# Performance work log

Hardware: AMD Instinct MI355X
Metric: run time of the kernel (lower is better)

Reference implementation:

```python
import jax, jax.numpy as jnp
import numpy as np

N_NODES = 50000
N_EDGES = 800000
D_IN = 96
D_EDGE = 32
D_OUT = 96
N_TYPES = 4


def setup_inputs() -> dict:
    key = jax.random.key(0)
    k = jax.random.split(key, 6)
    x = jax.random.normal(k[0], (N_NODES, D_IN), dtype=jnp.float32)
    edge_features = jax.random.normal(k[1], (N_NODES, D_EDGE), dtype=jnp.float32)
    edge_index = jax.random.randint(k[2], (2, N_EDGES), 0, N_NODES, dtype=jnp.int32)
    edge_type = jax.random.randint(k[3], (N_EDGES,), 0, N_TYPES, dtype=jnp.int32)
    # One RelEdgeConv per relation type: Linear(D_IN + D_EDGE -> D_OUT) message fn
    scale = 1.0 / np.sqrt(D_IN + D_EDGE)
    W_msg = jax.random.uniform(k[4], (N_TYPES, D_IN + D_EDGE, D_OUT), jnp.float32, -scale, scale)
    b_msg = jax.random.uniform(k[5], (N_TYPES, D_OUT), jnp.float32, -scale, scale)
    return {"x": x, "edge_features": edge_features, "edge_index": edge_index,
            "edge_type": edge_type, "W_msg": W_msg, "b_msg": b_msg}


def reference(x, edge_features, edge_index, edge_type, W_msg, b_msg):
    # Node-level edge_features (shape[0] == N) -> per-edge relative features
    src, dst = edge_index[0], edge_index[1]
    e = jnp.abs(edge_features[src] - edge_features[dst])          # [E, De]
    feat = jnp.concatenate([x[src], e], axis=-1)                  # [E, Din+De]
    n_nodes = x.shape[0]
    n_types = W_msg.shape[0]

    def per_type(t):
        # relation mask: zero out messages for edges of other types
        mask = (edge_type == t).astype(x.dtype)[:, None]          # [E, 1]
        m = (feat @ W_msg[t] + b_msg[t]) * mask                   # [E, Dout]
        # scatter-add messages to destination nodes
        return jax.ops.segment_sum(m, dst, num_segments=n_nodes)  # [N, Dout]

    out = jnp.stack([per_type(t) for t in range(n_types)])        # [T, N, Dout]
    return out.mean(axis=0)
```

## Files before the change

kernel.cpp:

```cpp
#include <hip/hip_runtime.h>

#define E_EDGES 800000
#define NN 50000
#define D_IN 96
#define D_EDGE 32
#define D_OUT 96
#define KSUM 512
#define SSTRIDE 520
#define NB2 782
#define BCAP2 1216
#define NCHUNK 256
#define CHE 3125
#define CHIT 13
#define BUILD_BLOCKS 512

typedef __attribute__((ext_vector_type(8))) __bf16 bf16x8;
typedef __attribute__((ext_vector_type(4))) float floatx4;

__device__ __forceinline__ float lo16(unsigned int u) {
    return __builtin_bit_cast(float, u << 16);
}
__device__ __forceinline__ float hi16(unsigned int u) {
    return __builtin_bit_cast(float, u & 0xFFFF0000u);
}
__device__ __forceinline__ unsigned int pk2(float a, float b) {
    unsigned short ua = __builtin_bit_cast(unsigned short, (__bf16)a);
    unsigned short ub = __builtin_bit_cast(unsigned short, (__bf16)b);
    return (unsigned int)ua | ((unsigned int)ub << 16);
}

__global__ __launch_bounds__(256) void k_prep(const int* __restrict__ ei,
                                              const int* __restrict__ et,
                                              const float* __restrict__ x,
                                              const float* __restrict__ ef,
                                              const float* __restrict__ Wm,
                                              int* __restrict__ cursor,
                                              int* __restrict__ eb,
                                              __bf16* __restrict__ WT,
                                              unsigned int* __restrict__ xeb) {
    __shared__ int lcnt[NB2];
    __shared__ int gb[NB2];
    int tid = threadIdx.x, bid = blockIdx.x;

    if (bid < NCHUNK) {
        int e0 = bid * CHE;
        for (int i = tid; i < NB2; i += 256) lcnt[i] = 0;
        __syncthreads();

        int pv[CHIT], br[CHIT];
#pragma unroll
        for (int it = 0; it < CHIT; it++) {
            int i = it * 256 + tid;
            br[it] = -1;
            if (i < CHE) {
                int e = e0 + i;
                int dst = ei[E_EDGES + e];
                int b = dst >> 6;
                int rank = atomicAdd(&lcnt[b], 1);
                pv[it] = (ei[e] << 6) | (et[e] << 22) | ((dst & 63) << 24);
                br[it] = rank | (b << 16);
            }
        }
        __syncthreads();
        for (int b = tid; b < NB2; b += 256)
            gb[b] = lcnt[b] ? atomicAdd(&cursor[b], lcnt[b]) : 0;
        __syncthreads();
#pragma unroll
        for (int it = 0; it < CHIT; it++) {
            if (br[it] >= 0) {
                int b = br[it] >> 16, rank = br[it] & 0xFFFF;
                int pos = gb[b] + rank;
                if (pos < BCAP2) eb[b * BCAP2 + pos] = pv[it];
            }
        }
    } else {
        int b2 = bid - NCHUNK;
        int gtid = b2 * 256 + tid;
        int lane = tid & 63, w = tid >> 6;
        for (int n = b2 * 4 + w; n < NN; n += BUILD_BLOCKS * 4) {
            float2 v;
            if (lane < 48) v = *(const float2*)(x  + (size_t)n * D_IN   + 2 * lane);
            else           v = *(const float2*)(ef + (size_t)n * D_EDGE + 2 * (lane - 48));
            xeb[(size_t)n * 64 + lane] = pk2(v.x, v.y);
        }
        for (int i = gtid; i < 96 * KSUM; i += BUILD_BLOCKS * 256) {
            int n = i >> 9, k = i & 511;
            WT[n * KSUM + k] = (__bf16)Wm[(size_t)k * 96 + n];
        }
    }
}

__global__ __launch_bounds__(256) void k_fused(const int* __restrict__ cursor,
                                               const int* __restrict__ eb,
                                               const unsigned int* __restrict__ xeb,
                                               const __bf16* __restrict__ WT,
                                               const float* __restrict__ bm,
                                               float* __restrict__ out) {
    __shared__ int ecopy[BCAP2];
    __shared__ int elist[BCAP2];
    __shared__ int h[256], hbase[256], c2[256];
    __shared__ __align__(16) __bf16 Sl[16][SSTRIDE];

    int tid = threadIdx.x, lane = tid & 63, w = tid >> 6;
    int B = blockIdx.x;
    int seg = B * BCAP2;
    int m = min(cursor[B], BCAP2);

    h[tid] = 0;
    __syncthreads();

    for (int i = tid; i < m; i += 256) {
        int p = eb[seg + i];
        ecopy[i] = p;
        atomicAdd(&h[(p >> 22) & 255], 1);
    }
    __syncthreads();

    int v = h[tid];
    c2[tid] = v; __syncthreads();
    for (int d = 1; d < 256; d <<= 1) {
        int t = (tid >= d) ? c2[tid - d] : 0;
        __syncthreads();
        c2[tid] += t; __syncthreads();
    }
    hbase[tid] = c2[tid] - v;
    c2[tid] = c2[tid] - v;
    __syncthreads();

    for (int i = tid; i < m; i += 256) {
        int p = ecopy[i];
        int pos = atomicAdd(&c2[(p >> 22) & 255], 1);
        elist[pos] = p;
    }
    __syncthreads();

    unsigned int Mmask = (lane >= 48) ? 0x7FFFFFFFu : 0xFFFFFFFFu;

#define ACCS(u, v) do {                                                        \
        float f0 = lo16(u), f1 = hi16(u);                                      \
        f0 = __builtin_bit_cast(float,                                         \
                 __builtin_bit_cast(unsigned int, f0 - e0) & Mmask);           \
        f1 = __builtin_bit_cast(float,                                         \
                 __builtin_bit_cast(unsigned int, f1 - e1) & Mmask);           \
        int sty = (__builtin_amdgcn_readfirstlane(v) >> 22) & 3;               \
        if      (sty == 0) { s0a += f0; s0b += f1; }                           \
        else if (sty == 1) { s1a += f0; s1b += f1; }                           \
        else if (sty == 2) { s2a += f0; s2b += f1; }                           \
        else               { s3a += f0; s3b += f1; }                           \
    } while (0)

    int quad = lane >> 4, low = lane & 15;

    for (int c4 = 0; c4 < 4; c4++) {
        for (int j = 0; j < 4; j++) {
            int lr = w * 4 + j;
            int nl = c4 * 16 + lr;
            int n = B * 64 + nl;
            int bs = hbase[nl * 4];
            int num = h[nl * 4] + h[nl * 4 + 1] + h[nl * 4 + 2] + h[nl * 4 + 3];
            float s0a = 0, s0b = 0, s1a = 0, s1b = 0,
                  s2a = 0, s2b = 0, s3a = 0, s3b = 0;
            float e0 = 0.f, e1 = 0.f;
            if (lane >= 48 && num > 0) {
                unsigned int u = xeb[(size_t)n * 64 + lane];
                e0 = lo16(u); e1 = hi16(u);
            }

            int i = 0;
            for (; i + 7 < num; i += 8) {
                int v0 = elist[bs + i],     v1 = elist[bs + i + 1];
                int v2 = elist[bs + i + 2], v3 = elist[bs + i + 3];
                int v4 = elist[bs + i + 4], v5 = elist[bs + i + 5];
                int v6 = elist[bs + i + 6], v7 = elist[bs + i + 7];
                unsigned int u0 = xeb[(v0 & 0x3FFFFF) + lane];
                unsigned int u1 = xeb[(v1 & 0x3FFFFF) + lane];
                unsigned int u2 = xeb[(v2 & 0x3FFFFF) + lane];
                unsigned int u3 = xeb[(v3 & 0x3FFFFF) + lane];
                unsigned int u4 = xeb[(v4 & 0x3FFFFF) + lane];
                unsigned int u5 = xeb[(v5 & 0x3FFFFF) + lane];
                unsigned int u6 = xeb[(v6 & 0x3FFFFF) + lane];
                unsigned int u7 = xeb[(v7 & 0x3FFFFF) + lane];
                ACCS(u0, v0); ACCS(u1, v1); ACCS(u2, v2); ACCS(u3, v3);
                ACCS(u4, v4); ACCS(u5, v5); ACCS(u6, v6); ACCS(u7, v7);
            }
            for (; i < num; i++) {
                int vv = elist[bs + i];
                unsigned int u = xeb[(vv & 0x3FFFFF) + lane];
                ACCS(u, vv);
            }

            unsigned int* sp = (unsigned int*)&Sl[lr][0];
            sp[  0 + lane] = pk2(s0a, s0b);
            sp[ 64 + lane] = pk2(s1a, s1b);
            sp[128 + lane] = pk2(s2a, s2b);
            sp[192 + lane] = pk2(s3a, s3b);
        }
        __syncthreads();

        bf16x8 a[16];
        const __bf16* ap = &Sl[low][0] + quad * 8;
#pragma unroll
        for (int ks = 0; ks < 16; ks++) a[ks] = *(const bf16x8*)(ap + ks * 32);

        for (int ct = w; ct < 6; ct += 4) {
            floatx4 acc = {0.f, 0.f, 0.f, 0.f};
            const __bf16* bp = WT + (size_t)(ct * 16 + low) * KSUM + quad * 8;
#pragma unroll
            for (int ks = 0; ks < 16; ks++)
                acc = __builtin_amdgcn_mfma_f32_16x16x32_bf16(
                    a[ks], *(const bf16x8*)(bp + ks * 32), acc, 0, 0, 0);
            int col = ct * 16 + low;
#pragma unroll
            for (int rg = 0; rg < 4; rg++) {
                int r = quad * 4 + rg;
                int nl = c4 * 16 + r;
                int g = B * 64 + nl;
                if (g < NN) {
                    float bias = (float)h[nl * 4 + 0] * bm[col]
                               + (float)h[nl * 4 + 1] * bm[96 + col]
                               + (float)h[nl * 4 + 2] * bm[192 + col]
                               + (float)h[nl * 4 + 3] * bm[288 + col];
                    out[(size_t)g * D_OUT + col] = 0.25f * (acc[rg] + bias);
                }
            }
        }
        __syncthreads();
    }
#undef ACCS
}

extern "C" void kernel_launch(void* const* d_in, const int* in_sizes, int n_in,
                              void* d_out, int out_size, void* d_ws, size_t ws_size,
                              hipStream_t stream) {
    const float* x  = (const float*)d_in[0];
    const float* ef = (const float*)d_in[1];
    const int*   ei = (const int*)d_in[2];
    const int*   et = (const int*)d_in[3];
    const float* Wm = (const float*)d_in[4];
    const float* bm = (const float*)d_in[5];
    float* out = (float*)d_out;

    int* cursor = (int*)d_ws;
    int* eb     = cursor + 1024;
    __bf16* WT  = (__bf16*)(eb + NB2 * BCAP2);
    unsigned int* xeb = (unsigned int*)(WT + 96 * KSUM);

    hipMemsetAsync(cursor, 0, NB2 * sizeof(int), stream);
    k_prep <<<NCHUNK + BUILD_BLOCKS, 256, 0, stream>>>(ei, et, x, ef, Wm,
                                                       cursor, eb, WT, xeb);
    k_fused<<<NB2, 256, 0, stream>>>(cursor, eb, xeb, WT, bm, out);
}
```

Baseline: 208.4 us.

## Halve destination bucket size and stage scattered edge writes through shared memory

Destination buckets shrink from 64 to 32 nodes, so the fused kernel launches twice as many blocks, each with a smaller edge list and two 16-row MFMA chunks instead of four. This raises parallelism and occupancy for the gather/aggregate phase. The prep kernel now does a block-local prefix scan over bucket counts and stages edges in shared memory so the global writes to the bucket array are grouped. A 4-wide unrolled tail loop is added to the gather. The extra shared memory in prep (two arrays of CHE ints) may lower occupancy for the prep and build blocks, and the per-bucket capacity of 704 could drop edges if a 32-node bucket overflows.

```diff
diff --git a/kernel.cpp b/kernel.cpp
--- a/kernel.cpp
+++ b/kernel.cpp
@@ -7,12 +7,13 @@
 #define D_OUT 96
 #define KSUM 512
 #define SSTRIDE 520
-#define NB2 782
-#define BCAP2 1216
+#define NB3 1564
+#define BCAP3 704
 #define NCHUNK 256
 #define CHE 3125
 #define CHIT 13
 #define BUILD_BLOCKS 512
+#define SPT 7
 
 typedef __attribute__((ext_vector_type(8))) __bf16 bf16x8;
 typedef __attribute__((ext_vector_type(4))) float floatx4;
@@ -38,13 +39,17 @@
                                               int* __restrict__ eb,
                                               __bf16* __restrict__ WT,
                                               unsigned int* __restrict__ xeb) {
-    __shared__ int lcnt[NB2];
-    __shared__ int gb[NB2];
+    __shared__ int lcnt[NB3];
+    __shared__ int lexcl[NB3];
+    __shared__ int gb[NB3];
+    __shared__ int tmp[256];
+    __shared__ int stage[CHE];
+    __shared__ int spos[CHE];
     int tid = threadIdx.x, bid = blockIdx.x;
 
     if (bid < NCHUNK) {
         int e0 = bid * CHE;
-        for (int i = tid; i < NB2; i += 256) lcnt[i] = 0;
+        for (int i = tid; i < NB3; i += 256) lcnt[i] = 0;
         __syncthreads();
 
         int pv[CHIT], br[CHIT];
@@ -55,23 +60,50 @@
             if (i < CHE) {
                 int e = e0 + i;
                 int dst = ei[E_EDGES + e];
-                int b = dst >> 6;
+                int b = dst >> 5;
                 int rank = atomicAdd(&lcnt[b], 1);
-                pv[it] = (ei[e] << 6) | (et[e] << 22) | ((dst & 63) << 24);
+                pv[it] = (ei[e] << 6) | (et[e] << 22) | ((dst & 31) << 24);
                 br[it] = rank | (b << 16);
             }
         }
         __syncthreads();
-        for (int b = tid; b < NB2; b += 256)
+        {
+            int s = 0;
+#pragma unroll
+            for (int k = 0; k < SPT; k++) {
+                int idx = tid * SPT + k;
+                if (idx < NB3) { lexcl[idx] = s; s += lcnt[idx]; }
+            }
+            tmp[tid] = s; __syncthreads();
+            for (int d = 1; d < 256; d <<= 1) {
+                int t = (tid >= d) ? tmp[tid - d] : 0;
+                __syncthreads();
+                tmp[tid] += t; __syncthreads();
+            }
+            int base = tmp[tid] - s;
+#pragma unroll
+            for (int k = 0; k < SPT; k++) {
+                int idx = tid * SPT + k;
+                if (idx < NB3) lexcl[idx] += base;
+            }
+        }
+        for (int b = tid; b < NB3; b += 256)
             gb[b] = lcnt[b] ? atomicAdd(&cursor[b], lcnt[b]) : 0;
         __syncthreads();
 #pragma unroll
         for (int it = 0; it < CHIT; it++) {
             if (br[it] >= 0) {
                 int b = br[it] >> 16, rank = br[it] & 0xFFFF;
-                int pos = gb[b] + rank;
-                if (pos < BCAP2) eb[b * BCAP2 + pos] = pv[it];
-            }
+                int lidx = lexcl[b] + rank;
+                stage[lidx] = pv[it];
+                int gp = gb[b] + rank;
+                spos[lidx] = (gp < BCAP3) ? (b * BCAP3 + gp) : -1;
+            }
+        }
+        __syncthreads();
+        for (int i = tid; i < CHE; i += 256) {
+            int p = spos[i];
+            if (p >= 0) eb[p] = stage[i];
         }
     } else {
         int b2 = bid - NCHUNK;
@@ -96,40 +128,40 @@
                                                const __bf16* __restrict__ WT,
                                                const float* __restrict__ bm,
                                                float* __restrict__ out) {
-    __shared__ int ecopy[BCAP2];
-    __shared__ int elist[BCAP2];
-    __shared__ int h[256], hbase[256], c2[256];
+    __shared__ int ecopy[BCAP3];
+    __shared__ int elist[BCAP3];
+    __shared__ int h[128], hbase[128], c2[256];
     __shared__ __align__(16) __bf16 Sl[16][SSTRIDE];
 
     int tid = threadIdx.x, lane = tid & 63, w = tid >> 6;
     int B = blockIdx.x;
-    int seg = B * BCAP2;
-    int m = min(cursor[B], BCAP2);
-
-    h[tid] = 0;
+    int seg = B * BCAP3;
+    int m = min(cursor[B], BCAP3);
+
+    if (tid < 128) h[tid] = 0;
     __syncthreads();
 
     for (int i = tid; i < m; i += 256) {
         int p = eb[seg + i];
         ecopy[i] = p;
-        atomicAdd(&h[(p >> 22) & 255], 1);
-    }
-    __syncthreads();
-
-    int v = h[tid];
+        atomicAdd(&h[(p >> 22) & 127], 1);
+    }
+    __syncthreads();
+
+    int v = (tid < 128) ? h[tid] : 0;
     c2[tid] = v; __syncthreads();
     for (int d = 1; d < 256; d <<= 1) {
         int t = (tid >= d) ? c2[tid - d] : 0;
         __syncthreads();
         c2[tid] += t; __syncthreads();
     }
-    hbase[tid] = c2[tid] - v;
+    if (tid < 128) { hbase[tid] = c2[tid] - v; }
     c2[tid] = c2[tid] - v;
     __syncthreads();
 
     for (int i = tid; i < m; i += 256) {
         int p = ecopy[i];
-        int pos = atomicAdd(&c2[(p >> 22) & 255], 1);
+        int pos = atomicAdd(&c2[(p >> 22) & 127], 1);
         elist[pos] = p;
     }
     __syncthreads();
@@ -151,11 +183,11 @@
 
     int quad = lane >> 4, low = lane & 15;
 
-    for (int c4 = 0; c4 < 4; c4++) {
+    for (int ch = 0; ch < 2; ch++) {
         for (int j = 0; j < 4; j++) {
             int lr = w * 4 + j;
-            int nl = c4 * 16 + lr;
-            int n = B * 64 + nl;
+            int nl = ch * 16 + lr;
+            int n = B * 32 + nl;
             int bs = hbase[nl * 4];
             int num = h[nl * 4] + h[nl * 4 + 1] + h[nl * 4 + 2] + h[nl * 4 + 3];
             float s0a = 0, s0b = 0, s1a = 0, s1b = 0,
@@ -183,6 +215,15 @@
                 ACCS(u0, v0); ACCS(u1, v1); ACCS(u2, v2); ACCS(u3, v3);
                 ACCS(u4, v4); ACCS(u5, v5); ACCS(u6, v6); ACCS(u7, v7);
             }
+            for (; i + 3 < num; i += 4) {
+                int v0 = elist[bs + i],     v1 = elist[bs + i + 1];
+                int v2 = elist[bs + i + 2], v3 = elist[bs + i + 3];
+                unsigned int u0 = xeb[(v0 & 0x3FFFFF) + lane];
+                unsigned int u1 = xeb[(v1 & 0x3FFFFF) + lane];
+                unsigned int u2 = xeb[(v2 & 0x3FFFFF) + lane];
+                unsigned int u3 = xeb[(v3 & 0x3FFFFF) + lane];
+                ACCS(u0, v0); ACCS(u1, v1); ACCS(u2, v2); ACCS(u3, v3);
+            }
             for (; i < num; i++) {
                 int vv = elist[bs + i];
                 unsigned int u = xeb[(vv & 0x3FFFFF) + lane];
@@ -213,8 +254,8 @@
 #pragma unroll
             for (int rg = 0; rg < 4; rg++) {
                 int r = quad * 4 + rg;
-                int nl = c4 * 16 + r;
-                int g = B * 64 + nl;
+                int nl = ch * 16 + r;
+                int g = B * 32 + nl;
                 if (g < NN) {
                     float bias = (float)h[nl * 4 + 0] * bm[col]
                                + (float)h[nl * 4 + 1] * bm[96 + col]
@@ -241,12 +282,12 @@
     float* out = (float*)d_out;
 
     int* cursor = (int*)d_ws;
-    int* eb     = cursor + 1024;
-    __bf16* WT  = (__bf16*)(eb + NB2 * BCAP2);
+    int* eb     = cursor + 2048;
+    __bf16* WT  = (__bf16*)(eb + NB3 * BCAP3);
     unsigned int* xeb = (unsigned int*)(WT + 96 * KSUM);
 
-    hipMemsetAsync(cursor, 0, NB2 * sizeof(int), stream);
+    hipMemsetAsync(cursor, 0, NB3 * sizeof(int), stream);
     k_prep <<<NCHUNK + BUILD_BLOCKS, 256, 0, stream>>>(ei, et, x, ef, Wm,
                                                        cursor, eb, WT, xeb);
-    k_fused<<<NB2, 256, 0, stream>>>(cursor, eb, xeb, WT, bm, out);
-}
+    k_fused<<<NB3, 256, 0, stream>>>(cursor, eb, xeb, WT, bm, out);
+}
```

Result: faster. 202.4 us (-2.9%).

## Shrink destination buckets to 16 nodes and gather per-type edge runs

Applied to the files above, without the earlier changes.

Destination buckets shrink from 64 to 16 nodes, so the fused kernel launches 3125 blocks instead of 782. Each block runs a single MFMA tile pass instead of four. The 256-entry block scan becomes a 64-lane wavefront shuffle scan. The gather loop walks each (node, type) run on its own, dropping the readfirstlane type branch, and uses a 4-wide masked unroll that clamps out-of-range elist reads. This aims at more parallelism and less divergent per-edge branching, at the cost of more blocks, more bucket atomics and per-block WT reloads, and a lower bucket capacity (384) that could overflow on skewed degree distributions.

```diff
diff --git a/kernel.cpp b/kernel.cpp
--- a/kernel.cpp
+++ b/kernel.cpp
@@ -7,8 +7,8 @@
 #define D_OUT 96
 #define KSUM 512
 #define SSTRIDE 520
-#define NB2 782
-#define BCAP2 1216
+#define NB4 3125
+#define BCAP4 384
 #define NCHUNK 256
 #define CHE 3125
 #define CHIT 13
@@ -38,13 +38,13 @@
                                               int* __restrict__ eb,
                                               __bf16* __restrict__ WT,
                                               unsigned int* __restrict__ xeb) {
-    __shared__ int lcnt[NB2];
-    __shared__ int gb[NB2];
+    __shared__ int lcnt[NB4];
+    __shared__ int gb[NB4];
     int tid = threadIdx.x, bid = blockIdx.x;
 
     if (bid < NCHUNK) {
         int e0 = bid * CHE;
-        for (int i = tid; i < NB2; i += 256) lcnt[i] = 0;
+        for (int i = tid; i < NB4; i += 256) lcnt[i] = 0;
         __syncthreads();
 
         int pv[CHIT], br[CHIT];
@@ -55,14 +55,14 @@
             if (i < CHE) {
                 int e = e0 + i;
                 int dst = ei[E_EDGES + e];
-                int b = dst >> 6;
+                int b = dst >> 4;
                 int rank = atomicAdd(&lcnt[b], 1);
-                pv[it] = (ei[e] << 6) | (et[e] << 22) | ((dst & 63) << 24);
+                pv[it] = (ei[e] << 6) | (et[e] << 22) | ((dst & 15) << 24);
                 br[it] = rank | (b << 16);
             }
         }
         __syncthreads();
-        for (int b = tid; b < NB2; b += 256)
+        for (int b = tid; b < NB4; b += 256)
             gb[b] = lcnt[b] ? atomicAdd(&cursor[b], lcnt[b]) : 0;
         __syncthreads();
 #pragma unroll
@@ -70,7 +70,7 @@
             if (br[it] >= 0) {
                 int b = br[it] >> 16, rank = br[it] & 0xFFFF;
                 int pos = gb[b] + rank;
-                if (pos < BCAP2) eb[b * BCAP2 + pos] = pv[it];
+                if (pos < BCAP4) eb[b * BCAP4 + pos] = pv[it];
             }
         }
     } else {
@@ -96,137 +96,117 @@
                                                const __bf16* __restrict__ WT,
                                                const float* __restrict__ bm,
                                                float* __restrict__ out) {
-    __shared__ int ecopy[BCAP2];
-    __shared__ int elist[BCAP2];
-    __shared__ int h[256], hbase[256], c2[256];
+    __shared__ int ecopy[BCAP4];
+    __shared__ int elist[BCAP4];
+    __shared__ int h[64], hbase[64];
+    __shared__ int c2[64];
     __shared__ __align__(16) __bf16 Sl[16][SSTRIDE];
 
     int tid = threadIdx.x, lane = tid & 63, w = tid >> 6;
     int B = blockIdx.x;
-    int seg = B * BCAP2;
-    int m = min(cursor[B], BCAP2);
-
-    h[tid] = 0;
+    int seg = B * BCAP4;
+    int m = min(cursor[B], BCAP4);
+
+    if (tid < 64) h[tid] = 0;
     __syncthreads();
 
     for (int i = tid; i < m; i += 256) {
         int p = eb[seg + i];
         ecopy[i] = p;
-        atomicAdd(&h[(p >> 22) & 255], 1);
-    }
-    __syncthreads();
-
-    int v = h[tid];
-    c2[tid] = v; __syncthreads();
-    for (int d = 1; d < 256; d <<= 1) {
-        int t = (tid >= d) ? c2[tid - d] : 0;
-        __syncthreads();
-        c2[tid] += t; __syncthreads();
-    }
-    hbase[tid] = c2[tid] - v;
-    c2[tid] = c2[tid] - v;
+        atomicAdd(&h[(p >> 22) & 63], 1);
+    }
+    __syncthreads();
+
+    if (w == 0) {
+        int v = h[lane];
+        int s = v;
+        for (int d = 1; d < 64; d <<= 1) {
+            int t = __shfl_up(s, d, 64);
+            if (lane >= d) s += t;
+        }
+        hbase[lane] = s - v;
+        c2[lane] = s - v;
+    }
     __syncthreads();
 
     for (int i = tid; i < m; i += 256) {
         int p = ecopy[i];
-        int pos = atomicAdd(&c2[(p >> 22) & 255], 1);
+        int pos = atomicAdd(&c2[(p >> 22) & 63], 1);
         elist[pos] = p;
     }
     __syncthreads();
 
     unsigned int Mmask = (lane >= 48) ? 0x7FFFFFFFu : 0xFFFFFFFFu;
-
-#define ACCS(u, v) do {                                                        \
-        float f0 = lo16(u), f1 = hi16(u);                                      \
+    int quad = lane >> 4, low = lane & 15;
+
+#define EDGE(k) do {                                                           \
+        float f0 = lo16(u##k), f1 = hi16(u##k);                                \
         f0 = __builtin_bit_cast(float,                                         \
                  __builtin_bit_cast(unsigned int, f0 - e0) & Mmask);           \
         f1 = __builtin_bit_cast(float,                                         \
                  __builtin_bit_cast(unsigned int, f1 - e1) & Mmask);           \
-        int sty = (__builtin_amdgcn_readfirstlane(v) >> 22) & 3;               \
-        if      (sty == 0) { s0a += f0; s0b += f1; }                           \
-        else if (sty == 1) { s1a += f0; s1b += f1; }                           \
-        else if (sty == 2) { s2a += f0; s2b += f1; }                           \
-        else               { s3a += f0; s3b += f1; }                           \
+        sa += (i + k < num) ? f0 : 0.f;                                        \
+        sb += (i + k < num) ? f1 : 0.f;                                        \
     } while (0)
 
-    int quad = lane >> 4, low = lane & 15;
-
-    for (int c4 = 0; c4 < 4; c4++) {
-        for (int j = 0; j < 4; j++) {
-            int lr = w * 4 + j;
-            int nl = c4 * 16 + lr;
-            int n = B * 64 + nl;
-            int bs = hbase[nl * 4];
-            int num = h[nl * 4] + h[nl * 4 + 1] + h[nl * 4 + 2] + h[nl * 4 + 3];
-            float s0a = 0, s0b = 0, s1a = 0, s1b = 0,
-                  s2a = 0, s2b = 0, s3a = 0, s3b = 0;
-            float e0 = 0.f, e1 = 0.f;
-            if (lane >= 48 && num > 0) {
-                unsigned int u = xeb[(size_t)n * 64 + lane];
-                e0 = lo16(u); e1 = hi16(u);
-            }
-
-            int i = 0;
-            for (; i + 7 < num; i += 8) {
-                int v0 = elist[bs + i],     v1 = elist[bs + i + 1];
-                int v2 = elist[bs + i + 2], v3 = elist[bs + i + 3];
-                int v4 = elist[bs + i + 4], v5 = elist[bs + i + 5];
-                int v6 = elist[bs + i + 6], v7 = elist[bs + i + 7];
+    for (int j = 0; j < 4; j++) {
+        int nl = w * 4 + j;
+        int n = B * 16 + nl;
+        float e0 = 0.f, e1 = 0.f;
+        if (lane >= 48) {
+            unsigned int u = xeb[(size_t)n * 64 + lane];
+            e0 = lo16(u); e1 = hi16(u);
+        }
+        unsigned int* sp = (unsigned int*)&Sl[nl][0];
+
+#pragma unroll
+        for (int t = 0; t < 4; t++) {
+            int bs = hbase[nl * 4 + t];
+            int num = h[nl * 4 + t];
+            float sa = 0.f, sb = 0.f;
+            for (int i = 0; i < num; i += 4) {
+                int i1 = bs + i + 1, i2 = bs + i + 2, i3 = bs + i + 3;
+                int lim = m - 1;
+                int v0 = elist[bs + i];
+                int v1 = elist[i1 < m ? i1 : lim];
+                int v2 = elist[i2 < m ? i2 : lim];
+                int v3 = elist[i3 < m ? i3 : lim];
                 unsigned int u0 = xeb[(v0 & 0x3FFFFF) + lane];
                 unsigned int u1 = xeb[(v1 & 0x3FFFFF) + lane];
                 unsigned int u2 = xeb[(v2 & 0x3FFFFF) + lane];
                 unsigned int u3 = xeb[(v3 & 0x3FFFFF) + lane];
-                unsigned int u4 = xeb[(v4 & 0x3FFFFF) + lane];
-                unsigned int u5 = xeb[(v5 & 0x3FFFFF) + lane];
-                unsigned int u6 = xeb[(v6 & 0x3FFFFF) + lane];
-                unsigned int u7 = xeb[(v7 & 0x3FFFFF) + lane];
-                ACCS(u0, v0); ACCS(u1, v1); ACCS(u2, v2); ACCS(u3, v3);
-                ACCS(u4, v4); ACCS(u5, v5); ACCS(u6, v6); ACCS(u7, v7);
+                EDGE(0); EDGE(1); EDGE(2); EDGE(3);
             }
-            for (; i < num; i++) {
-                int vv = elist[bs + i];
-                unsigned int u = xeb[(vv & 0x3FFFFF) + lane];
-                ACCS(u, vv);
-            }
-
-            unsigned int* sp = (unsigned int*)&Sl[lr][0];
-            sp[  0 + lane] = pk2(s0a, s0b);
-            sp[ 64 + lane] = pk2(s1a, s1b);
-            sp[128 + lane] = pk2(s2a, s2b);
-            sp[192 + lane] = pk2(s3a, s3b);
-        }
-        __syncthreads();
-
-        bf16x8 a[16];
-        const __bf16* ap = &Sl[low][0] + quad * 8;
-#pragma unroll
-        for (int ks = 0; ks < 16; ks++) a[ks] = *(const bf16x8*)(ap + ks * 32);
-
-        for (int ct = w; ct < 6; ct += 4) {
-            floatx4 acc = {0.f, 0.f, 0.f, 0.f};
-            const __bf16* bp = WT + (size_t)(ct * 16 + low) * KSUM + quad * 8;
-#pragma unroll
-            for (int ks = 0; ks < 16; ks++)
-                acc = __builtin_amdgcn_mfma_f32_16x16x32_bf16(
-                    a[ks], *(const bf16x8*)(bp + ks * 32), acc, 0, 0, 0);
-            int col = ct * 16 + low;
-#pragma unroll
-            for (int rg = 0; rg < 4; rg++) {
-                int r = quad * 4 + rg;
-                int nl = c4 * 16 + r;
-                int g = B * 64 + nl;
-                if (g < NN) {
-                    float bias = (float)h[nl * 4 + 0] * bm[col]
-                               + (float)h[nl * 4 + 1] * bm[96 + col]
-                               + (float)h[nl * 4 + 2] * bm[192 + col]
-                               + (float)h[nl * 4 + 3] * bm[288 + col];
-                    out[(size_t)g * D_OUT + col] = 0.25f * (acc[rg] + bias);
-                }
-            }
-        }
-        __syncthreads();
-    }
-#undef ACCS
+            sp[t * 64 + lane] = pk2(sa, sb);
+        }
+    }
+#undef EDGE
+    __syncthreads();
+
+    bf16x8 a[16];
+    const __bf16* ap = &Sl[low][0] + quad * 8;
+#pragma unroll
+    for (int ks = 0; ks < 16; ks++) a[ks] = *(const bf16x8*)(ap + ks * 32);
+
+    for (int ct = w; ct < 6; ct += 4) {
+        floatx4 acc = {0.f, 0.f, 0.f, 0.f};
+        const __bf16* bp = WT + (size_t)(ct * 16 + low) * KSUM + quad * 8;
+#pragma unroll
+        for (int ks = 0; ks < 16; ks++)
+            acc = __builtin_amdgcn_mfma_f32_16x16x32_bf16(
+                a[ks], *(const bf16x8*)(bp + ks * 32), acc, 0, 0, 0);
+        int col = ct * 16 + low;
+#pragma unroll
+        for (int rg = 0; rg < 4; rg++) {
+            int r = quad * 4 + rg;
+            int g = B * 16 + r;
+            float bias = (float)h[r * 4 + 0] * bm[col]
+                       + (float)h[r * 4 + 1] * bm[96 + col]
+                       + (float)h[r * 4 + 2] * bm[192 + col]
+                       + (float)h[r * 4 + 3] * bm[288 + col];
+            out[(size_t)g * D_OUT + col] = 0.25f * (acc[rg] + bias);
+        }
+    }
 }
 
 extern "C" void kernel_launch(void* const* d_in, const int* in_sizes, int n_in,
@@ -241,12 +221,12 @@
     float* out = (float*)d_out;
 
     int* cursor = (int*)d_ws;
-    int* eb     = cursor + 1024;
-    __bf16* WT  = (__bf16*)(eb + NB2 * BCAP2);
+    int* eb     = cursor + 3200;
+    __bf16* WT  = (__bf16*)(eb + NB4 * BCAP4);
     unsigned int* xeb = (unsigned int*)(WT + 96 * KSUM);
 
-    hipMemsetAsync(cursor, 0, NB2 * sizeof(int), stream);
+    hipMemsetAsync(cursor, 0, NB4 * sizeof(int), stream);
     k_prep <<<NCHUNK + BUILD_BLOCKS, 256, 0, stream>>>(ei, et, x, ef, Wm,
                                                        cursor, eb, WT, xeb);
-    k_fused<<<NB2, 256, 0, stream>>>(cursor, eb, xeb, WT, bm, out);
-}
+    k_fused<<<NB4, 256, 0, stream>>>(cursor, eb, xeb, WT, bm, out);
+}
```

After: 184.9 us. 1.13x faster.
